# Performance work log

Hardware: AMD Instinct MI355X
Metric: run time of the kernel (lower is better)

## Reference

```python
import jax, jax.numpy as jnp
import numpy as np

N_NODES = 50000
N_EDGES = 800000
D_IN, D_HID, D_OUT = 128, 128, 64
BN_EPS = 1e-5


def gcn_conv(x, W, b, src, dst, ew, n):
    # PyG GCNConv: out[i] = sum_j norm_ij * (x @ W)[j] + b, with self-loops added
    xw = x @ W                                   # [N, D_out]
    loop = jnp.arange(n)
    s = jnp.concatenate([src, loop])             # add self-loops (weight 1)
    d = jnp.concatenate([dst, loop])
    w = jnp.concatenate([ew, jnp.ones((n,), x.dtype)])
    deg = jax.ops.segment_sum(w, d, num_segments=n)
    dinv = jnp.where(deg > 0, jax.lax.rsqrt(deg), 0.0)
    norm = dinv[s] * w * dinv[d]                 # symmetric normalization
    msg = xw[s] * norm[:, None]                  # gather + scale  [E+N, D_out]
    return jax.ops.segment_sum(msg, d, num_segments=n) + b


def setup_inputs() -> dict:
    key = jax.random.key(0)
    ks = jax.random.split(key, 12)
    x = jax.random.normal(ks[0], (N_NODES, D_IN), dtype=jnp.float32)
    edge_index = jax.random.randint(ks[1], (2, N_EDGES), 0, N_NODES, dtype=jnp.int64)
    edge_weight = jax.random.uniform(ks[2], (N_EDGES,), dtype=jnp.float32)
    W1 = jax.random.normal(ks[3], (D_IN, D_HID), dtype=jnp.float32) * 0.05
    b1 = jnp.zeros((D_HID,), jnp.float32)
    gamma = jnp.ones((D_HID,), jnp.float32)
    beta = jnp.zeros((D_HID,), jnp.float32)
    running_mean = jax.random.normal(ks[4], (D_HID,), dtype=jnp.float32) * 0.1
    running_var = jax.random.uniform(ks[5], (D_HID,), dtype=jnp.float32) + 0.5
    W2 = jax.random.normal(ks[6], (D_HID, D_OUT), dtype=jnp.float32) * 0.05
    b2 = jnp.zeros((D_OUT,), jnp.float32)
    return {"x": x, "edge_index": edge_index, "edge_weight": edge_weight,
            "W1": W1, "b1": b1, "gamma": gamma, "beta": beta,
            "running_mean": running_mean, "running_var": running_var,
            "W2": W2, "b2": b2}


def reference(x, edge_index, edge_weight, W1, b1, gamma, beta,
              running_mean, running_var, W2, b2):
    src, dst = edge_index[0], edge_index[1]
    n = x.shape[0]
    h = gcn_conv(x, W1, b1, src, dst, edge_weight, n)
    # BatchNorm1d in eval mode (running stats); dropout inactive in eval
    h = (h - running_mean) * jax.lax.rsqrt(running_var + BN_EPS) * gamma + beta
    h = jax.nn.relu(h)
    out = gcn_conv(h, W2, b2, src, dst, edge_weight, n)
    return out
```

## Files before the change

kernel.cpp:

```cpp
#include <hip/hip_runtime.h>
#include <hip/hip_fp16.h>

#define BN_EPS 1e-5f
#define PAD 64
#define CAP 4608

typedef __attribute__((ext_vector_type(8))) short short8;
typedef __attribute__((ext_vector_type(4))) float f32x4;

static __device__ __forceinline__ unsigned short f2bf(float f) {
    unsigned u = __float_as_uint(f);
    u += 0x7FFF + ((u >> 16) & 1);
    return (unsigned short)(u >> 16);
}
static __device__ __forceinline__ float bf2f(unsigned short b) {
    return __uint_as_float((unsigned)b << 16);
}
static __device__ __forceinline__ unsigned pk(int s, float w) {
    return ((unsigned)s << 16) | (unsigned)__half_as_ushort(__float2half_rn(w));
}
static __device__ __forceinline__ float pw(unsigned e) {
    return __half2float(__ushort_as_half((unsigned short)(e & 0xFFFFu)));
}

__global__ __launch_bounds__(256) void k_fused(const int* __restrict__ src, const int* __restrict__ dst,
                                               const float* __restrict__ ew,
                                               uint2* __restrict__ bins, int* __restrict__ gcnt,
                                               int e, int gfill, int stride, int nb,
                                               const float* __restrict__ A, const float* __restrict__ W,
                                               unsigned short* __restrict__ C, int n,
                                               const float* __restrict__ b1, const float* __restrict__ gamma,
                                               const float* __restrict__ beta, const float* __restrict__ mean,
                                               const float* __restrict__ var,
                                               float* __restrict__ bnscale, float* __restrict__ bnshift,
                                               const float* __restrict__ W2, unsigned short* __restrict__ w2bf) {
    __shared__ unsigned short W1s[16384];
    int tid = threadIdx.x;
    int b = (int)blockIdx.x;
    int gGemm = (n + 63) / 64;

    bool isFill = ((b % stride) == 0) && (b / stride < gfill);
    if (isFill) {
        int* lcnt  = (int*)W1s;
        int* gbase = lcnt + 256;
        lcnt[tid] = 0;
        __syncthreads();

        int i0 = ((b / stride) * 256 + tid) * 8;
        unsigned pv[8];  int bk[8]; int rk[8]; unsigned dl[8];
        int cnt8 = 0;
        if (i0 + 7 < e) {
            int4   s0 = *(const int4*)(src + i0), s1 = *(const int4*)(src + i0 + 4);
            int4   d0 = *(const int4*)(dst + i0), d1 = *(const int4*)(dst + i0 + 4);
            float4 w0 = *(const float4*)(ew + i0), w1 = *(const float4*)(ew + i0 + 4);
            int   ss[8] = {s0.x, s0.y, s0.z, s0.w, s1.x, s1.y, s1.z, s1.w};
            int   dd[8] = {d0.x, d0.y, d0.z, d0.w, d1.x, d1.y, d1.z, d1.w};
            float ww[8] = {w0.x, w0.y, w0.z, w0.w, w1.x, w1.y, w1.z, w1.w};
            #pragma unroll
            for (int j = 0; j < 8; ++j) {
                int d_ = dd[j];
                bk[j] = d_ >> 8;
                dl[j] = (unsigned)(d_ & 255);
                rk[j] = atomicAdd(&lcnt[bk[j]], 1);
                pv[j] = pk(ss[j], ww[j]);
            }
            cnt8 = 8;
        } else {
            for (int j = 0; j < 8; ++j) {
                int i = i0 + j;
                if (i < e) {
                    int d_ = dst[i];
                    bk[j] = d_ >> 8;
                    dl[j] = (unsigned)(d_ & 255);
                    rk[j] = atomicAdd(&lcnt[bk[j]], 1);
                    pv[j] = pk(src[i], ew[i]);
                    cnt8 = j + 1;
                }
            }
        }
        __syncthreads();
        if (tid < nb) gbase[tid] = atomicAdd(&gcnt[tid], lcnt[tid]);
        __syncthreads();
        for (int j = 0; j < cnt8; ++j) {
            int pos = gbase[bk[j]] + rk[j];
            if (pos < CAP) bins[(size_t)bk[j] * CAP + pos] = make_uint2(pv[j], dl[j]);
        }
        return;
    }

    int fillsBefore = (b == 0) ? 0 : min(gfill, (b - 1) / stride + 1);
    int g = b - fillsBefore;
    if (g == gGemm) {
        if (tid < 128) {
            float sc = gamma[tid] * rsqrtf(var[tid] + BN_EPS);
            bnscale[tid] = sc;
            bnshift[tid] = (b1[tid] - mean[tid]) * sc + beta[tid];
        }
        const float4* W4 = (const float4*)W2;
        ushort4* O = (ushort4*)w2bf;
        #pragma unroll
        for (int q = 0; q < 8; ++q) {
            float4 v = W4[q * 256 + tid];
            O[q * 256 + tid] = make_ushort4(f2bf(v.x), f2bf(v.y), f2bf(v.z), f2bf(v.w));
        }
        return;
    }

    int row0 = g * 64;

    {
        int k  = tid >> 1;
        int c0 = (tid & 1) * 64;
        int kk = k >> 5, lg = (k >> 3) & 3, ii = k & 7;
        int tbase = kk * 4096 + lg * 128 + ii;
        const float4* Wr = (const float4*)(W + (size_t)k * 128 + c0);
        #pragma unroll
        for (int j = 0; j < 16; ++j) {
            float4 v = Wr[j];
            int n0 = c0 + j * 4;
            W1s[tbase + ((n0 + 0) >> 4) * 512 + ((n0 + 0) & 15) * 8] = f2bf(v.x);
            W1s[tbase + ((n0 + 1) >> 4) * 512 + ((n0 + 1) & 15) * 8] = f2bf(v.y);
            W1s[tbase + ((n0 + 2) >> 4) * 512 + ((n0 + 2) & 15) * 8] = f2bf(v.z);
            W1s[tbase + ((n0 + 3) >> 4) * 512 + ((n0 + 3) & 15) * 8] = f2bf(v.w);
        }
    }
    __syncthreads();

    int w = tid >> 6, lane = tid & 63;
    int arow = row0 + w * 16 + (lane & 15);
    if (arow > n - 1) arow = n - 1;
    const float* xrow = A + (size_t)arow * 128 + ((lane >> 4) * 8);
    const unsigned short* Wl = W1s + (size_t)lane * 8;

    f32x4 z = {0.f, 0.f, 0.f, 0.f};
    f32x4 acc0 = z, acc1 = z, acc2 = z, acc3 = z, acc4 = z, acc5 = z, acc6 = z, acc7 = z;

    #pragma unroll
    for (int kk = 0; kk < 4; ++kk) {
        float4 v0 = *(const float4*)(xrow + kk * 32);
        float4 v1 = *(const float4*)(xrow + kk * 32 + 4);
        short8 a;
        a[0] = (short)f2bf(v0.x); a[1] = (short)f2bf(v0.y);
        a[2] = (short)f2bf(v0.z); a[3] = (short)f2bf(v0.w);
        a[4] = (short)f2bf(v1.x); a[5] = (short)f2bf(v1.y);
        a[6] = (short)f2bf(v1.z); a[7] = (short)f2bf(v1.w);
        const unsigned short* Wk = Wl + kk * 4096;
        short8 b0 = *(const short8*)(Wk);
        short8 b1 = *(const short8*)(Wk + 512);
        short8 b2 = *(const short8*)(Wk + 1024);
        short8 b3 = *(const short8*)(Wk + 1536);
        short8 b4 = *(const short8*)(Wk + 2048);
        short8 b5 = *(const short8*)(Wk + 2560);
        short8 b6 = *(const short8*)(Wk + 3072);
        short8 b7 = *(const short8*)(Wk + 3584);
        acc0 = __builtin_amdgcn_mfma_f32_16x16x32_bf16(a, b0, acc0, 0, 0, 0);
        acc1 = __builtin_amdgcn_mfma_f32_16x16x32_bf16(a, b1, acc1, 0, 0, 0);
        acc2 = __builtin_amdgcn_mfma_f32_16x16x32_bf16(a, b2, acc2, 0, 0, 0);
        acc3 = __builtin_amdgcn_mfma_f32_16x16x32_bf16(a, b3, acc3, 0, 0, 0);
        acc4 = __builtin_amdgcn_mfma_f32_16x16x32_bf16(a, b4, acc4, 0, 0, 0);
        acc5 = __builtin_amdgcn_mfma_f32_16x16x32_bf16(a, b5, acc5, 0, 0, 0);
        acc6 = __builtin_amdgcn_mfma_f32_16x16x32_bf16(a, b6, acc6, 0, 0, 0);
        acc7 = __builtin_amdgcn_mfma_f32_16x16x32_bf16(a, b7, acc7, 0, 0, 0);
    }

    int rw = row0 + w * 16 + ((lane >> 4) << 2);
    int cb = lane & 15;
    #define STORE_NT(av, nt)                                                              \
        if (rw + 0 < n) C[(size_t)(rw + 0) * 128 + (nt)*16 + cb] = f2bf(av[0]);           \
        if (rw + 1 < n) C[(size_t)(rw + 1) * 128 + (nt)*16 + cb] = f2bf(av[1]);           \
        if (rw + 2 < n) C[(size_t)(rw + 2) * 128 + (nt)*16 + cb] = f2bf(av[2]);           \
        if (rw + 3 < n) C[(size_t)(rw + 3) * 128 + (nt)*16 + cb] = f2bf(av[3]);
    STORE_NT(acc0, 0) STORE_NT(acc1, 1) STORE_NT(acc2, 2) STORE_NT(acc3, 3)
    STORE_NT(acc4, 4) STORE_NT(acc5, 5) STORE_NT(acc6, 6) STORE_NT(acc7, 7)
    #undef STORE_NT
}

__global__ __launch_bounds__(256) void k_csr(const uint2* __restrict__ bins, const int* __restrict__ gcnt,
                                             unsigned* __restrict__ pad, int* __restrict__ cnt,
                                             float* __restrict__ dinv, int n) {
    __shared__ unsigned csr[256 * PAD];
    __shared__ int lc[256];
    int tid = threadIdx.x;
    int b = (int)blockIdx.x;
    int node0 = b << 8;
    int nodes = min(256, n - node0);
    lc[tid] = 0;
    __syncthreads();

    int m = gcnt[b];
    if (m > CAP) m = CAP;
    const uint2* seg = bins + (size_t)b * CAP;
    for (int i = tid; i < m; i += 256) {
        uint2 v = seg[i];
        int r = atomicAdd(&lc[v.y], 1);
        if (r < PAD) csr[v.y * PAD + r] = v.x;
    }
    __syncthreads();

    if (tid < nodes) {
        int c = lc[tid];
        cnt[node0 + tid] = c;
        int cc = min(c, PAD);
        float s = 1.0f;
        for (int p = 0; p < cc; ++p) s += pw(csr[tid * PAD + p]);
        dinv[node0 + tid] = rsqrtf(s);
    }
    const uint4* s4 = (const uint4*)csr;
    uint4* d4 = (uint4*)(pad + (size_t)node0 * PAD);
    int tot = nodes * (PAD / 4);
    for (int q = tid; q < tot; q += 256) d4[q] = s4[q];
}

__global__ __launch_bounds__(256) void k_ag12(const unsigned short* __restrict__ xw, const int* __restrict__ cnt,
                                              const unsigned* __restrict__ pad,
                                              const float* __restrict__ dinv,
                                              const float* __restrict__ scale, const float* __restrict__ shift,
                                              const unsigned short* __restrict__ w2bf,
                                              unsigned short* __restrict__ hw2, int n) {
    __shared__ unsigned short W2s[128 * 64];
    int tid = threadIdx.x;
    {
        const uint4* s4 = (const uint4*)w2bf;
        uint4* d4 = (uint4*)W2s;
        #pragma unroll
        for (int q = 0; q < 4; ++q) d4[q * 256 + tid] = s4[q * 256 + tid];
    }
    __syncthreads();

    int g = tid >> 5;
    int lc = tid & 31;
    int node = blockIdx.x * 8 + g;
    if (node >= n) return;

    unsigned hu0, hu1;
    {
        const ushort4* X4 = (const ushort4*)xw;
        float di = dinv[node];
        int c = min(cnt[node], PAD);
        size_t base = (size_t)node * PAD;
        ushort4 q0 = X4[(size_t)node * 32 + lc];
        float4 acc0 = make_float4(bf2f(q0.x) * di, bf2f(q0.y) * di, bf2f(q0.z) * di, bf2f(q0.w) * di);
        float4 acc1 = make_float4(0, 0, 0, 0);
        float4 acc2 = make_float4(0, 0, 0, 0);
        float4 acc3 = make_float4(0, 0, 0, 0);
        int p = 0;
        for (; p + 3 < c; p += 4) {
            uint4 ee = *(const uint4*)(pad + base + p);
            float w0 = pw(ee.x) * dinv[ee.x >> 16];
            float w1 = pw(ee.y) * dinv[ee.y >> 16];
            float w2 = pw(ee.z) * dinv[ee.z >> 16];
            float w3 = pw(ee.w) * dinv[ee.w >> 16];
            ushort4 a = X4[(size_t)(ee.x >> 16) * 32 + lc];
            ushort4 b = X4[(size_t)(ee.y >> 16) * 32 + lc];
            ushort4 gg = X4[(size_t)(ee.z >> 16) * 32 + lc];
            ushort4 d = X4[(size_t)(ee.w >> 16) * 32 + lc];
            acc0.x += w0 * bf2f(a.x); acc0.y += w0 * bf2f(a.y); acc0.z += w0 * bf2f(a.z); acc0.w += w0 * bf2f(a.w);
            acc1.x += w1 * bf2f(b.x); acc1.y += w1 * bf2f(b.y); acc1.z += w1 * bf2f(b.z); acc1.w += w1 * bf2f(b.w);
            acc2.x += w2 * bf2f(gg.x); acc2.y += w2 * bf2f(gg.y); acc2.z += w2 * bf2f(gg.z); acc2.w += w2 * bf2f(gg.w);
            acc3.x += w3 * bf2f(d.x); acc3.y += w3 * bf2f(d.y); acc3.z += w3 * bf2f(d.z); acc3.w += w3 * bf2f(d.w);
        }
        for (; p < c; ++p) {
            unsigned e0 = pad[base + p];
            float w0 = pw(e0) * dinv[e0 >> 16];
            ushort4 a = X4[(size_t)(e0 >> 16) * 32 + lc];
            acc0.x += w0 * bf2f(a.x); acc0.y += w0 * bf2f(a.y); acc0.z += w0 * bf2f(a.z); acc0.w += w0 * bf2f(a.w);
        }
        acc0.x = (acc0.x + acc1.x + acc2.x + acc3.x) * di;
        acc0.y = (acc0.y + acc1.y + acc2.y + acc3.y) * di;
        acc0.z = (acc0.z + acc1.z + acc2.z + acc3.z) * di;
        acc0.w = (acc0.w + acc1.w + acc2.w + acc3.w) * di;
        float4 Sc = ((const float4*)scale)[lc];
        float4 Sh = ((const float4*)shift)[lc];
        unsigned short r0 = f2bf(fmaxf(acc0.x * Sc.x + Sh.x, 0.0f));
        unsigned short r1 = f2bf(fmaxf(acc0.y * Sc.y + Sh.y, 0.0f));
        unsigned short r2 = f2bf(fmaxf(acc0.z * Sc.z + Sh.z, 0.0f));
        unsigned short r3 = f2bf(fmaxf(acc0.w * Sc.w + Sh.w, 0.0f));
        hu0 = ((unsigned)r1 << 16) | (unsigned)r0;
        hu1 = ((unsigned)r3 << 16) | (unsigned)r2;
    }

    float a0 = 0.0f, a1 = 0.0f;
    const unsigned* W2u = (const unsigned*)W2s;
    #pragma unroll 8
    for (int k = 0; k < 32; ++k) {
        unsigned p0 = (unsigned)__shfl((int)hu0, k, 32);
        unsigned p1 = (unsigned)__shfl((int)hu1, k, 32);
        float h0 = bf2f((unsigned short)(p0 & 0xFFFFu));
        float h1 = bf2f((unsigned short)(p0 >> 16));
        float h2 = bf2f((unsigned short)(p1 & 0xFFFFu));
        float h3 = bf2f((unsigned short)(p1 >> 16));
        unsigned w0u = W2u[(4 * k + 0) * 32 + lc];
        unsigned w1u = W2u[(4 * k + 1) * 32 + lc];
        unsigned w2u = W2u[(4 * k + 2) * 32 + lc];
        unsigned w3u = W2u[(4 * k + 3) * 32 + lc];
        a0 += h0 * bf2f((unsigned short)(w0u & 0xFFFFu));
        a1 += h0 * bf2f((unsigned short)(w0u >> 16));
        a0 += h1 * bf2f((unsigned short)(w1u & 0xFFFFu));
        a1 += h1 * bf2f((unsigned short)(w1u >> 16));
        a0 += h2 * bf2f((unsigned short)(w2u & 0xFFFFu));
        a1 += h2 * bf2f((unsigned short)(w2u >> 16));
        a0 += h3 * bf2f((unsigned short)(w3u & 0xFFFFu));
        a1 += h3 * bf2f((unsigned short)(w3u >> 16));
    }
    unsigned outp = ((unsigned)f2bf(a1) << 16) | (unsigned)f2bf(a0);
    ((unsigned*)hw2)[(size_t)node * 32 + lc] = outp;
}

__global__ __launch_bounds__(256) void k_agg2(const unsigned short* __restrict__ hw, const int* __restrict__ cnt,
                                              const unsigned* __restrict__ pad,
                                              const float* __restrict__ dinv,
                                              const float* __restrict__ b2, float* __restrict__ out, int n) {
    int node = blockIdx.x * 16 + (threadIdx.x >> 4);
    if (node >= n) return;
    int lc = threadIdx.x & 15;
    const ushort4* X4 = (const ushort4*)hw;
    float di = dinv[node];
    int c = min(cnt[node], PAD);
    size_t base = (size_t)node * PAD;
    ushort4 q0 = X4[(size_t)node * 16 + lc];
    float4 acc0 = make_float4(bf2f(q0.x) * di, bf2f(q0.y) * di, bf2f(q0.z) * di, bf2f(q0.w) * di);
    float4 acc1 = make_float4(0, 0, 0, 0);
    float4 acc2 = make_float4(0, 0, 0, 0);
    float4 acc3 = make_float4(0, 0, 0, 0);
    int p = 0;
    for (; p + 3 < c; p += 4) {
        uint4 ee = *(const uint4*)(pad + base + p);
        float w0 = pw(ee.x) * dinv[ee.x >> 16];
        float w1 = pw(ee.y) * dinv[ee.y >> 16];
        float w2 = pw(ee.z) * dinv[ee.z >> 16];
        float w3 = pw(ee.w) * dinv[ee.w >> 16];
        ushort4 a = X4[(size_t)(ee.x >> 16) * 16 + lc];
        ushort4 b = X4[(size_t)(ee.y >> 16) * 16 + lc];
        ushort4 g = X4[(size_t)(ee.z >> 16) * 16 + lc];
        ushort4 d = X4[(size_t)(ee.w >> 16) * 16 + lc];
        acc0.x += w0 * bf2f(a.x); acc0.y += w0 * bf2f(a.y); acc0.z += w0 * bf2f(a.z); acc0.w += w0 * bf2f(a.w);
        acc1.x += w1 * bf2f(b.x); acc1.y += w1 * bf2f(b.y); acc1.z += w1 * bf2f(b.z); acc1.w += w1 * bf2f(b.w);
        acc2.x += w2 * bf2f(g.x); acc2.y += w2 * bf2f(g.y); acc2.z += w2 * bf2f(g.z); acc2.w += w2 * bf2f(g.w);
        acc3.x += w3 * bf2f(d.x); acc3.y += w3 * bf2f(d.y); acc3.z += w3 * bf2f(d.z); acc3.w += w3 * bf2f(d.w);
    }
    for (; p < c; ++p) {
        unsigned e0 = pad[base + p];
        float w0 = pw(e0) * dinv[e0 >> 16];
        ushort4 a = X4[(size_t)(e0 >> 16) * 16 + lc];
        acc0.x += w0 * bf2f(a.x); acc0.y += w0 * bf2f(a.y); acc0.z += w0 * bf2f(a.z); acc0.w += w0 * bf2f(a.w);
    }
    float4 B = ((const float4*)b2)[lc];
    acc0.x = (acc0.x + acc1.x + acc2.x + acc3.x) * di + B.x;
    acc0.y = (acc0.y + acc1.y + acc2.y + acc3.y) * di + B.y;
    acc0.z = (acc0.z + acc1.z + acc2.z + acc3.z) * di + B.z;
    acc0.w = (acc0.w + acc1.w + acc2.w + acc3.w) * di + B.w;
    ((float4*)out)[(size_t)node * 16 + lc] = acc0;
}


extern "C" void kernel_launch(void* const* d_in, const int* in_sizes, int n_in,
                              void* d_out, int out_size, void* d_ws, size_t ws_size,
                              hipStream_t stream) {
    const float* x     = (const float*)d_in[0];
    const int*   ei    = (const int*)d_in[1];
    const float* ew    = (const float*)d_in[2];
    const float* W1    = (const float*)d_in[3];
    const float* b1    = (const float*)d_in[4];
    const float* gamma = (const float*)d_in[5];
    const float* beta  = (const float*)d_in[6];
    const float* rmean = (const float*)d_in[7];
    const float* rvar  = (const float*)d_in[8];
    const float* W2    = (const float*)d_in[9];
    const float* b2    = (const float*)d_in[10];
    float* out = (float*)d_out;

    int N = in_sizes[0] / 128;
    int E = in_sizes[2];
    const int* src = ei;
    const int* dst = ei + E;
    int NB = (N + 255) >> 8;

    char* p = (char*)d_ws;
    auto carve = [&](size_t bytes) { char* q = p; p += (bytes + 255) & ~(size_t)255; return (void*)q; };
    int*      cnt     = (int*)     carve(sizeof(int) * (size_t)N);
    unsigned* pad     = (unsigned*)carve(sizeof(unsigned) * (size_t)N * PAD);
    float*    dinv    = (float*)   carve(sizeof(float) * (size_t)N);
    float*    bnscale = (float*)   carve(sizeof(float) * 128);
    float*    bnshift = (float*)   carve(sizeof(float) * 128);
    unsigned short* w2bf = (unsigned short*)carve(sizeof(unsigned short) * 128 * 64);
    unsigned short* xw1  = (unsigned short*)carve(sizeof(unsigned short) * (size_t)N * 128);
    unsigned short* hw2  = (unsigned short*)carve(sizeof(unsigned short) * (size_t)N * 64);
    int*      gcnt    = (int*)     carve(sizeof(int) * (size_t)NB);
    uint2*    bins    = (uint2*)   carve(sizeof(uint2) * (size_t)NB * CAP);

    int gFill = (E + 2047) / 2048;
    int gGemm = (N + 63) / 64;
    int T     = gFill + gGemm + 1;
    int S     = T / gFill;
    if (S < 2) S = 2;

    hipMemsetAsync(gcnt, 0, sizeof(int) * (size_t)NB, stream);
    k_fused <<<T, 256, 0, stream>>>(src, dst, ew, bins, gcnt, E, gFill, S, NB,
                                    x, W1, xw1, N,
                                    b1, gamma, beta, rmean, rvar, bnscale, bnshift,
                                    W2, w2bf);
    k_csr   <<<NB, 256, 0, stream>>>(bins, gcnt, pad, cnt, dinv, N);
    k_ag12  <<<(N + 7) / 8, 256, 0, stream>>>(xw1, cnt, pad, dinv, bnscale, bnshift, w2bf, hw2, N);
    k_agg2  <<<(N + 15) / 16, 256, 0, stream>>>(hw2, cnt, pad, dinv, b2, out, N);
}
```

Baseline: 193.0 us.

## Use MFMA for the fused second-layer GEMM with 32 nodes per block

The fused aggregation plus W2 projection kernel now processes 32 nodes per block: it aggregates rows into a swizzled LDS tile and then computes the 32x128 by 128x64 product with bf16 MFMA instructions, replacing the shuffle-based scalar FMA loop. W2 is pre-packed into the MFMA B-operand layout in the setup block. This is meant to cut ALU and shuffle cost and amortise the W2 LDS load over more nodes. In exchange the grid shrinks, only two of four waves run the MFMA phase, and partial rows are zero-filled only implicitly.

```diff
diff --git a/kernel.cpp b/kernel.cpp
--- a/kernel.cpp
+++ b/kernel.cpp
@@ -96,12 +96,23 @@
             bnscale[tid] = sc;
             bnshift[tid] = (b1[tid] - mean[tid]) * sc + beta[tid];
         }
-        const float4* W4 = (const float4*)W2;
-        ushort4* O = (ushort4*)w2bf;
         #pragma unroll
-        for (int q = 0; q < 8; ++q) {
-            float4 v = W4[q * 256 + tid];
-            O[q * 256 + tid] = make_ushort4(f2bf(v.x), f2bf(v.y), f2bf(v.z), f2bf(v.w));
+        for (int q = 0; q < 4; ++q) {
+            int s = tid * 4 + q;
+            int kk = s >> 8, nt = (s >> 6) & 3, lane = s & 63;
+            int kb = kk * 32 + ((lane >> 4) << 3);
+            int nc = (nt << 4) + (lane & 15);
+            ushort4 o0, o1;
+            o0.x = f2bf(W2[(kb + 0) * 64 + nc]);
+            o0.y = f2bf(W2[(kb + 1) * 64 + nc]);
+            o0.z = f2bf(W2[(kb + 2) * 64 + nc]);
+            o0.w = f2bf(W2[(kb + 3) * 64 + nc]);
+            o1.x = f2bf(W2[(kb + 4) * 64 + nc]);
+            o1.y = f2bf(W2[(kb + 5) * 64 + nc]);
+            o1.z = f2bf(W2[(kb + 6) * 64 + nc]);
+            o1.w = f2bf(W2[(kb + 7) * 64 + nc]);
+            ((ushort4*)w2bf)[s * 2]     = o0;
+            ((ushort4*)w2bf)[s * 2 + 1] = o1;
         }
         return;
     }
@@ -217,93 +228,104 @@
                                               const float* __restrict__ scale, const float* __restrict__ shift,
                                               const unsigned short* __restrict__ w2bf,
                                               unsigned short* __restrict__ hw2, int n) {
-    __shared__ unsigned short W2s[128 * 64];
+    __shared__ unsigned hs[32 * 64];
+    __shared__ unsigned short W2f[8192];
     int tid = threadIdx.x;
     {
         const uint4* s4 = (const uint4*)w2bf;
-        uint4* d4 = (uint4*)W2s;
+        uint4* d4 = (uint4*)W2f;
         #pragma unroll
         for (int q = 0; q < 4; ++q) d4[q * 256 + tid] = s4[q * 256 + tid];
     }
+
+    int grp = tid >> 5;
+    int lc  = tid & 31;
+    float4 Sc = ((const float4*)scale)[lc];
+    float4 Sh = ((const float4*)shift)[lc];
+    const ushort4* X4 = (const ushort4*)xw;
+    int node0 = (int)blockIdx.x * 32;
+
+    #pragma unroll 1
+    for (int r = 0; r < 4; ++r) {
+        int lrow = r * 8 + grp;
+        int node = node0 + lrow;
+        if (node < n) {
+            float di = dinv[node];
+            int c = min(cnt[node], PAD);
+            size_t base = (size_t)node * PAD;
+            ushort4 q0 = X4[(size_t)node * 32 + lc];
+            float4 acc0 = make_float4(bf2f(q0.x) * di, bf2f(q0.y) * di, bf2f(q0.z) * di, bf2f(q0.w) * di);
+            float4 acc1 = make_float4(0, 0, 0, 0);
+            float4 acc2 = make_float4(0, 0, 0, 0);
+            float4 acc3 = make_float4(0, 0, 0, 0);
+            int p = 0;
+            for (; p + 3 < c; p += 4) {
+                uint4 ee = *(const uint4*)(pad + base + p);
+                float w0 = pw(ee.x) * dinv[ee.x >> 16];
+                float w1 = pw(ee.y) * dinv[ee.y >> 16];
+                float w2 = pw(ee.z) * dinv[ee.z >> 16];
+                float w3 = pw(ee.w) * dinv[ee.w >> 16];
+                ushort4 a = X4[(size_t)(ee.x >> 16) * 32 + lc];
+                ushort4 b = X4[(size_t)(ee.y >> 16) * 32 + lc];
+                ushort4 gg = X4[(size_t)(ee.z >> 16) * 32 + lc];
+                ushort4 d = X4[(size_t)(ee.w >> 16) * 32 + lc];
+                acc0.x += w0 * bf2f(a.x); acc0.y += w0 * bf2f(a.y); acc0.z += w0 * bf2f(a.z); acc0.w += w0 * bf2f(a.w);
+                acc1.x += w1 * bf2f(b.x); acc1.y += w1 * bf2f(b.y); acc1.z += w1 * bf2f(b.z); acc1.w += w1 * bf2f(b.w);
+                acc2.x += w2 * bf2f(gg.x); acc2.y += w2 * bf2f(gg.y); acc2.z += w2 * bf2f(gg.z); acc2.w += w2 * bf2f(gg.w);
+                acc3.x += w3 * bf2f(d.x); acc3.y += w3 * bf2f(d.y); acc3.z += w3 * bf2f(d.z); acc3.w += w3 * bf2f(d.w);
+            }
+            for (; p < c; ++p) {
+                unsigned e0 = pad[base + p];
+                float w0 = pw(e0) * dinv[e0 >> 16];
+                ushort4 a = X4[(size_t)(e0 >> 16) * 32 + lc];
+                acc0.x += w0 * bf2f(a.x); acc0.y += w0 * bf2f(a.y); acc0.z += w0 * bf2f(a.z); acc0.w += w0 * bf2f(a.w);
+            }
+            acc0.x = (acc0.x + acc1.x + acc2.x + acc3.x) * di;
+            acc0.y = (acc0.y + acc1.y + acc2.y + acc3.y) * di;
+            acc0.z = (acc0.z + acc1.z + acc2.z + acc3.z) * di;
+            acc0.w = (acc0.w + acc1.w + acc2.w + acc3.w) * di;
+            unsigned short r0 = f2bf(fmaxf(acc0.x * Sc.x + Sh.x, 0.0f));
+            unsigned short r1 = f2bf(fmaxf(acc0.y * Sc.y + Sh.y, 0.0f));
+            unsigned short r2 = f2bf(fmaxf(acc0.z * Sc.z + Sh.z, 0.0f));
+            unsigned short r3 = f2bf(fmaxf(acc0.w * Sc.w + Sh.w, 0.0f));
+            unsigned hu0 = ((unsigned)r1 << 16) | (unsigned)r0;
+            unsigned hu1 = ((unsigned)r3 << 16) | (unsigned)r2;
+            unsigned byte = (unsigned)(lrow * 256 + lc * 8) ^ (unsigned)((lrow & 7) << 4);
+            *(uint2*)((char*)hs + byte) = make_uint2(hu0, hu1);
+        }
+    }
     __syncthreads();
 
-    int g = tid >> 5;
-    int lc = tid & 31;
-    int node = blockIdx.x * 8 + g;
-    if (node >= n) return;
-
-    unsigned hu0, hu1;
-    {
-        const ushort4* X4 = (const ushort4*)xw;
-        float di = dinv[node];
-        int c = min(cnt[node], PAD);
-        size_t base = (size_t)node * PAD;
-        ushort4 q0 = X4[(size_t)node * 32 + lc];
-        float4 acc0 = make_float4(bf2f(q0.x) * di, bf2f(q0.y) * di, bf2f(q0.z) * di, bf2f(q0.w) * di);
-        float4 acc1 = make_float4(0, 0, 0, 0);
-        float4 acc2 = make_float4(0, 0, 0, 0);
-        float4 acc3 = make_float4(0, 0, 0, 0);
-        int p = 0;
-        for (; p + 3 < c; p += 4) {
-            uint4 ee = *(const uint4*)(pad + base + p);
-            float w0 = pw(ee.x) * dinv[ee.x >> 16];
-            float w1 = pw(ee.y) * dinv[ee.y >> 16];
-            float w2 = pw(ee.z) * dinv[ee.z >> 16];
-            float w3 = pw(ee.w) * dinv[ee.w >> 16];
-            ushort4 a = X4[(size_t)(ee.x >> 16) * 32 + lc];
-            ushort4 b = X4[(size_t)(ee.y >> 16) * 32 + lc];
-            ushort4 gg = X4[(size_t)(ee.z >> 16) * 32 + lc];
-            ushort4 d = X4[(size_t)(ee.w >> 16) * 32 + lc];
-            acc0.x += w0 * bf2f(a.x); acc0.y += w0 * bf2f(a.y); acc0.z += w0 * bf2f(a.z); acc0.w += w0 * bf2f(a.w);
-            acc1.x += w1 * bf2f(b.x); acc1.y += w1 * bf2f(b.y); acc1.z += w1 * bf2f(b.z); acc1.w += w1 * bf2f(b.w);
-            acc2.x += w2 * bf2f(gg.x); acc2.y += w2 * bf2f(gg.y); acc2.z += w2 * bf2f(gg.z); acc2.w += w2 * bf2f(gg.w);
-            acc3.x += w3 * bf2f(d.x); acc3.y += w3 * bf2f(d.y); acc3.z += w3 * bf2f(d.z); acc3.w += w3 * bf2f(d.w);
-        }
-        for (; p < c; ++p) {
-            unsigned e0 = pad[base + p];
-            float w0 = pw(e0) * dinv[e0 >> 16];
-            ushort4 a = X4[(size_t)(e0 >> 16) * 32 + lc];
-            acc0.x += w0 * bf2f(a.x); acc0.y += w0 * bf2f(a.y); acc0.z += w0 * bf2f(a.z); acc0.w += w0 * bf2f(a.w);
-        }
-        acc0.x = (acc0.x + acc1.x + acc2.x + acc3.x) * di;
-        acc0.y = (acc0.y + acc1.y + acc2.y + acc3.y) * di;
-        acc0.z = (acc0.z + acc1.z + acc2.z + acc3.z) * di;
-        acc0.w = (acc0.w + acc1.w + acc2.w + acc3.w) * di;
-        float4 Sc = ((const float4*)scale)[lc];
-        float4 Sh = ((const float4*)shift)[lc];
-        unsigned short r0 = f2bf(fmaxf(acc0.x * Sc.x + Sh.x, 0.0f));
-        unsigned short r1 = f2bf(fmaxf(acc0.y * Sc.y + Sh.y, 0.0f));
-        unsigned short r2 = f2bf(fmaxf(acc0.z * Sc.z + Sh.z, 0.0f));
-        unsigned short r3 = f2bf(fmaxf(acc0.w * Sc.w + Sh.w, 0.0f));
-        hu0 = ((unsigned)r1 << 16) | (unsigned)r0;
-        hu1 = ((unsigned)r3 << 16) | (unsigned)r2;
-    }
-
-    float a0 = 0.0f, a1 = 0.0f;
-    const unsigned* W2u = (const unsigned*)W2s;
-    #pragma unroll 8
-    for (int k = 0; k < 32; ++k) {
-        unsigned p0 = (unsigned)__shfl((int)hu0, k, 32);
-        unsigned p1 = (unsigned)__shfl((int)hu1, k, 32);
-        float h0 = bf2f((unsigned short)(p0 & 0xFFFFu));
-        float h1 = bf2f((unsigned short)(p0 >> 16));
-        float h2 = bf2f((unsigned short)(p1 & 0xFFFFu));
-        float h3 = bf2f((unsigned short)(p1 >> 16));
-        unsigned w0u = W2u[(4 * k + 0) * 32 + lc];
-        unsigned w1u = W2u[(4 * k + 1) * 32 + lc];
-        unsigned w2u = W2u[(4 * k + 2) * 32 + lc];
-        unsigned w3u = W2u[(4 * k + 3) * 32 + lc];
-        a0 += h0 * bf2f((unsigned short)(w0u & 0xFFFFu));
-        a1 += h0 * bf2f((unsigned short)(w0u >> 16));
-        a0 += h1 * bf2f((unsigned short)(w1u & 0xFFFFu));
-        a1 += h1 * bf2f((unsigned short)(w1u >> 16));
-        a0 += h2 * bf2f((unsigned short)(w2u & 0xFFFFu));
-        a1 += h2 * bf2f((unsigned short)(w2u >> 16));
-        a0 += h3 * bf2f((unsigned short)(w3u & 0xFFFFu));
-        a1 += h3 * bf2f((unsigned short)(w3u >> 16));
-    }
-    unsigned outp = ((unsigned)f2bf(a1) << 16) | (unsigned)f2bf(a0);
-    ((unsigned*)hw2)[(size_t)node * 32 + lc] = outp;
+    int w = tid >> 6, lane = tid & 63;
+    if (w < 2) {
+        int ra = w * 16 + (lane & 15);
+        unsigned swz = (unsigned)((ra & 7) << 4);
+        f32x4 z = {0.f, 0.f, 0.f, 0.f};
+        f32x4 acc0 = z, acc1 = z, acc2 = z, acc3 = z;
+        #pragma unroll
+        for (int kk = 0; kk < 4; ++kk) {
+            unsigned byte = (unsigned)(ra * 256 + kk * 64 + ((lane >> 4) << 4)) ^ swz;
+            short8 a = *(const short8*)((const char*)hs + byte);
+            const unsigned short* Wk = W2f + kk * 2048 + (size_t)lane * 8;
+            short8 b0 = *(const short8*)(Wk);
+            short8 b1 = *(const short8*)(Wk + 512);
+            short8 b2 = *(const short8*)(Wk + 1024);
+            short8 b3 = *(const short8*)(Wk + 1536);
+            acc0 = __builtin_amdgcn_mfma_f32_16x16x32_bf16(a, b0, acc0, 0, 0, 0);
+            acc1 = __builtin_amdgcn_mfma_f32_16x16x32_bf16(a, b1, acc1, 0, 0, 0);
+            acc2 = __builtin_amdgcn_mfma_f32_16x16x32_bf16(a, b2, acc2, 0, 0, 0);
+            acc3 = __builtin_amdgcn_mfma_f32_16x16x32_bf16(a, b3, acc3, 0, 0, 0);
+        }
+        int rw = node0 + w * 16 + ((lane >> 4) << 2);
+        int cb = lane & 15;
+        #define ST_NT(av, nt)                                                                 \
+            if (rw + 0 < n) hw2[(size_t)(rw + 0) * 64 + (nt)*16 + cb] = f2bf(av[0]);          \
+            if (rw + 1 < n) hw2[(size_t)(rw + 1) * 64 + (nt)*16 + cb] = f2bf(av[1]);          \
+            if (rw + 2 < n) hw2[(size_t)(rw + 2) * 64 + (nt)*16 + cb] = f2bf(av[2]);          \
+            if (rw + 3 < n) hw2[(size_t)(rw + 3) * 64 + (nt)*16 + cb] = f2bf(av[3]);
+        ST_NT(acc0, 0) ST_NT(acc1, 1) ST_NT(acc2, 2) ST_NT(acc3, 3)
+        #undef ST_NT
+    }
 }
 
 __global__ __launch_bounds__(256) void k_agg2(const unsigned short* __restrict__ hw, const int* __restrict__ cnt,
@@ -400,6 +422,6 @@
                                     b1, gamma, beta, rmean, rvar, bnscale, bnshift,
                                     W2, w2bf);
     k_csr   <<<NB, 256, 0, stream>>>(bins, gcnt, pad, cnt, dinv, N);
-    k_ag12  <<<(N + 7) / 8, 256, 0, stream>>>(xw1, cnt, pad, dinv, bnscale, bnshift, w2bf, hw2, N);
+    k_ag12  <<<(N + 31) / 32, 256, 0, stream>>>(xw1, cnt, pad, dinv, bnscale, bnshift, w2bf, hw2, N);
     k_agg2  <<<(N + 15) / 16, 256, 0, stream>>>(hw2, cnt, pad, dinv, b2, out, N);
 }
```

After: 189.1 us. 1.02x faster.
